# Optimization experiments

Measured on AMD Instinct MI355X. Metric: run time of the kernel, lower is better.

Reference implementation:

```python
import jax, jax.numpy as jnp
import numpy as np

L, D, H, M, NC = 12, 768, 12, 3072, 1000
P, IMG, C = 16, 224, 3
HD = D // H // 2  # 32: diff-attn head dim (2*H query heads of HD, H value heads of 2*HD)
B = 32
N = (IMG // P) ** 2 + 1  # 197
EPS = 1e-5


def _layernorm(x, s, b):
    mu = x.mean(-1, keepdims=True)
    var = ((x - mu) ** 2).mean(-1, keepdims=True)
    return (x - mu) * jax.lax.rsqrt(var + EPS) * s + b


def _rmsnorm(x, s):
    ms = (x * x).mean(-1, keepdims=True)
    return x * jax.lax.rsqrt(ms + EPS) * s


def _diff_attn(x, qw, kw, vw, ow, lq1, lk1, lq2, lk2, sls, lam_init):
    b, n, _ = x.shape
    q = (x @ qw).reshape(b, n, 2 * H, HD)
    k = (x @ kw).reshape(b, n, 2 * H, HD)
    v = (x @ vw).reshape(b, n, H, 2 * HD)
    scores = jnp.einsum('bnhd,bmhd->bhnm', q, k) * (HD ** -0.5)
    attn = jax.nn.softmax(scores, axis=-1)  # [b, 2H, n, n]
    lam = jnp.exp(jnp.sum(lq1 * lk1)) - jnp.exp(jnp.sum(lq2 * lk2)) + lam_init
    attn = attn.reshape(b, H, 2, n, n)
    attn = attn[:, :, 0] - lam * attn[:, :, 1]  # differential attention map
    out = jnp.einsum('bhnm,bmhd->bnhd', attn, v)  # [b, n, H, 2*HD]
    out = _rmsnorm(out, sls) * (1.0 - lam_init)
    return out.reshape(b, n, D) @ ow


def _forward(x, conv_w, conv_b, cls_token, pos_emb,
             ln1_s, ln1_b, q_w, k_w, v_w, o_w, lq1, lk1, lq2, lk2, subln_s,
             ln2_s, ln2_b, w1, b1, w2, b2, lnf_s, lnf_b, head_w, head_b):
    # patch embed: conv stride=patch, then flatten to tokens
    h = jax.lax.conv_general_dilated(x, conv_w, (P, P), 'VALID',
                                     dimension_numbers=('NCHW', 'OIHW', 'NCHW'))
    h = h + conv_b[None, :, None, None]
    bsz = x.shape[0]
    h = h.reshape(bsz, D, -1).transpose(0, 2, 1)  # [B, 196, D]
    h = jnp.concatenate([jnp.broadcast_to(cls_token, (bsz, 1, D)), h], axis=1)
    h = h + pos_emb
    for i in range(L):
        lam_init = 0.8 - 0.6 * np.exp(-0.3 * i)
        a = _diff_attn(_layernorm(h, ln1_s[i], ln1_b[i]), q_w[i], k_w[i], v_w[i], o_w[i],
                       lq1[i], lk1[i], lq2[i], lk2[i], subln_s[i], lam_init)
        h = h + a
        m = _layernorm(h, ln2_s[i], ln2_b[i])
        m = jax.nn.gelu(m @ w1[i] + b1[i]) @ w2[i] + b2[i]
        h = h + m
    h = _layernorm(h, lnf_s, lnf_b)
    return h[:, 0] @ head_w + head_b


def setup_inputs() -> dict:
    key = jax.random.key(0)
    ks = iter(jax.random.split(key, 40))
    def rn(shape, s=0.02):
        return jax.random.normal(next(ks), shape, jnp.float32) * s
    return {
        'x': jax.random.normal(next(ks), (B, C, IMG, IMG), jnp.float32),
        'conv_w': rn((D, C, P, P)), 'conv_b': jnp.zeros((D,), jnp.float32),
        'cls_token': jnp.zeros((1, 1, D), jnp.float32),
        'pos_emb': rn((1, N, D)),
        'ln1_s': jnp.ones((L, D), jnp.float32), 'ln1_b': jnp.zeros((L, D), jnp.float32),
        'q_w': rn((L, D, D)), 'k_w': rn((L, D, D)), 'v_w': rn((L, D, D)), 'o_w': rn((L, D, D)),
        'lq1': rn((L, HD), 0.1), 'lk1': rn((L, HD), 0.1),
        'lq2': rn((L, HD), 0.1), 'lk2': rn((L, HD), 0.1),
        'subln_s': jnp.ones((L, 2 * HD), jnp.float32),
        'ln2_s': jnp.ones((L, D), jnp.float32), 'ln2_b': jnp.zeros((L, D), jnp.float32),
        'w1': rn((L, D, M)), 'b1': jnp.zeros((L, M), jnp.float32),
        'w2': rn((L, M, D)), 'b2': jnp.zeros((L, D), jnp.float32),
        'lnf_s': jnp.ones((D,), jnp.float32), 'lnf_b': jnp.zeros((D,), jnp.float32),
        'head_w': rn((D, NC)), 'head_b': jnp.zeros((NC,), jnp.float32),
    }


def reference(x, conv_w, conv_b, cls_token, pos_emb,
              ln1_s, ln1_b, q_w, k_w, v_w, o_w, lq1, lk1, lq2, lk2, subln_s,
              ln2_s, ln2_b, w1, b1, w2, b2, lnf_s, lnf_b, head_w, head_b):
    return _forward(x, conv_w, conv_b, cls_token, pos_emb,
                    ln1_s, ln1_b, q_w, k_w, v_w, o_w, lq1, lk1, lq2, lk2, subln_s,
                    ln2_s, ln2_b, w1, b1, w2, b2, lnf_s, lnf_b, head_w, head_b)
```

## Files before the change

kernel.cpp:

```cpp
#include <hip/hip_runtime.h>
#include <cmath>


typedef unsigned short u16;
typedef u16 u16x4 __attribute__((ext_vector_type(4)));
typedef u16 u16x8 __attribute__((ext_vector_type(8)));
typedef float fx4 __attribute__((ext_vector_type(4)));
typedef __bf16 bf16x8 __attribute__((ext_vector_type(8)));

#define MROWS 6304
#define MPAD  6400

__device__ __forceinline__ float bf2f(u16 u) {
  union { unsigned int i; float f; } c; c.i = ((unsigned int)u) << 16; return c.f;
}
__device__ __forceinline__ u16 f2bf(float f) {
  union { float f; unsigned int i; } c; c.f = f;
  return (u16)((c.i + 0x7FFFu + ((c.i >> 16) & 1u)) >> 16);
}
__device__ __forceinline__ float gelu_f(float x) {
  float u = 0.7978845608028654f * (x + 0.044715f * x * x * x);
  u = fminf(fmaxf(u, -30.f), 30.f);
  float e = __expf(2.f * u);
  return 0.5f * x * (1.f + (e - 1.f) / (e + 1.f));
}

__device__ __forceinline__ void gload16(const void* g, void* l) {
  __builtin_amdgcn_global_load_lds(
      (const __attribute__((address_space(1))) void*)g,
      (__attribute__((address_space(3))) void*)l, 16, 0, 0);
}

enum { EP_F32 = 0, EP_BF16 = 1, EP_GELU_BF16 = 2, EP_RESID_F32 = 3 };

template<int MODE, bool BIAS>
__global__ __launch_bounds__(256)
void gemm_bf16(const u16* __restrict__ A, const u16* __restrict__ Bt,
               const float* __restrict__ bias, const float* __restrict__ resid,
               void* __restrict__ outp, int M, int N, int K)
{
  __shared__ unsigned char lds[2 * 128 * 64 * 2];
  unsigned char* As = lds;
  unsigned char* Bs = lds + 128 * 64 * 2;
  const int tid = threadIdx.x;
  const int lane = tid & 63, w = tid >> 6;
  const int g = lane >> 4, l = lane & 15;
  const int wr = w >> 1, wc = w & 1;
  const int bm = blockIdx.x * 128, bn = blockIdx.y * 128;

  const int swz_half = ((lane & 7) ^ ((lane >> 3) & 7)) << 3;
  const int srow = 32 * w + (lane >> 3);
  const u16* gA = A + (size_t)(bm + srow) * K + swz_half;
  const u16* gB = Bt + (size_t)(bn + srow) * K + swz_half;
  unsigned char* lA = As + srow * 128 + ((lane & 7) << 4) - (size_t)lane * 16;
  unsigned char* lB = lA + (Bs - As);

  fx4 acc[4][4] = {};

  for (int kt = 0; kt < K; kt += 64) {
    #pragma unroll
    for (int c = 0; c < 4; ++c) {
      gload16(gA + (size_t)(8 * c) * K + kt, lA + (8 * c) * 128);
      gload16(gB + (size_t)(8 * c) * K + kt, lB + (8 * c) * 128);
    }
    __syncthreads();
    #pragma unroll
    for (int kk = 0; kk < 2; ++kk) {
      bf16x8 af[4], bfr[4];
      #pragma unroll
      for (int i = 0; i < 4; ++i) {
        int ar = wr * 64 + i * 16 + l;
        af[i] = *(const bf16x8*)(As + ar * 128 + ((kk * 64 + g * 16) ^ ((ar & 7) << 4)));
        int br = wc * 64 + i * 16 + l;
        bfr[i] = *(const bf16x8*)(Bs + br * 128 + ((kk * 64 + g * 16) ^ ((br & 7) << 4)));
      }
      #pragma unroll
      for (int i = 0; i < 4; ++i)
        #pragma unroll
        for (int j = 0; j < 4; ++j)
          acc[i][j] = __builtin_amdgcn_mfma_f32_16x16x32_bf16(af[i], bfr[j], acc[i][j], 0, 0, 0);
    }
    __syncthreads();
  }
  #pragma unroll
  for (int j = 0; j < 4; ++j) {
    int n = bn + wc * 64 + j * 16 + l;
    float bv = 0.f;
    if (BIAS) bv = bias[n];
    #pragma unroll
    for (int i = 0; i < 4; ++i) {
      int mbase = bm + wr * 64 + i * 16 + g * 4;
      #pragma unroll
      for (int q = 0; q < 4; ++q) {
        int m = mbase + q;
        if (m < M) {
          float v = acc[i][j][q] + bv;
          if (MODE == EP_GELU_BF16) {
            ((u16*)outp)[(size_t)m * N + n] = f2bf(gelu_f(v));
          } else if (MODE == EP_BF16) {
            ((u16*)outp)[(size_t)m * N + n] = f2bf(v);
          } else if (MODE == EP_RESID_F32) {
            ((float*)outp)[(size_t)m * N + n] = resid[(size_t)m * N + n] + v;
          } else {
            ((float*)outp)[(size_t)m * N + n] = v;
          }
        }
      }
    }
  }
}

template<bool OUTF32>
__global__ __launch_bounds__(64)
void layernorm_k(const float* __restrict__ x, const float* __restrict__ s,
                 const float* __restrict__ b, void* __restrict__ outp, size_t in_rstride)
{
  int r = blockIdx.x, lane = threadIdx.x;
  const fx4* xp = (const fx4*)(x + (size_t)r * in_rstride);
  fx4 v[3];
  float sum = 0.f, sq = 0.f;
  #pragma unroll
  for (int j = 0; j < 3; ++j) {
    v[j] = xp[j * 64 + lane];
    #pragma unroll
    for (int e = 0; e < 4; ++e) { sum += v[j][e]; sq += v[j][e] * v[j][e]; }
  }
  #pragma unroll
  for (int off = 32; off; off >>= 1) { sum += __shfl_xor(sum, off); sq += __shfl_xor(sq, off); }
  float mu = sum * (1.f / 768.f);
  float var = sq * (1.f / 768.f) - mu * mu;
  float rs = rsqrtf(var + 1e-5f);
  const fx4* sp = (const fx4*)s;
  const fx4* bp = (const fx4*)b;
  #pragma unroll
  for (int j = 0; j < 3; ++j) {
    fx4 sv = sp[j * 64 + lane], bv = bp[j * 64 + lane];
    if (OUTF32) {
      fx4 o;
      #pragma unroll
      for (int e = 0; e < 4; ++e) o[e] = (v[j][e] - mu) * rs * sv[e] + bv[e];
      *(fx4*)((float*)outp + (size_t)r * 768 + (j * 64 + lane) * 4) = o;
    } else {
      u16x4 o;
      #pragma unroll
      for (int e = 0; e < 4; ++e) o[e] = f2bf((v[j][e] - mu) * rs * sv[e] + bv[e]);
      *(u16x4*)((u16*)outp + (size_t)r * 768 + (j * 64 + lane) * 4) = o;
    }
  }
}

#define KSTR 40
#define VSTR 232
#define DA_LDS (2 * 224 * KSTR * 2 + 64 * VSTR * 2 + 4 * 16 * VSTR * 2)

__global__ __launch_bounds__(256)
void diff_attn(const u16* __restrict__ qkv, const float* __restrict__ lam_p,
               const float* __restrict__ sls, u16* __restrict__ outp, float lam_init)
{
  extern __shared__ char smem[];
  u16* K1s = (u16*)smem;
  u16* K2s = K1s + 224 * KSTR;
  u16* Vt  = K2s + 224 * KSTR;
  const int tid = threadIdx.x;
  const int w = tid >> 6, lane = tid & 63;
  const int g = lane >> 4, l = lane & 15;
  u16* Pw = Vt + 64 * VSTR + w * 16 * VSTR;

  const int bh = blockIdx.x;
  const int b = bh / 12, hh = bh % 12;
  const u16* base = qkv + (size_t)b * 197 * 2304;

  if (tid < 197) {
    const u16* kr = base + (size_t)tid * 2304 + 768 + hh * 64;
    *(u16x8*)(K1s + tid * KSTR + 0)  = *(const u16x8*)(kr + 0);
    *(u16x8*)(K1s + tid * KSTR + 8)  = *(const u16x8*)(kr + 8);
    *(u16x8*)(K1s + tid * KSTR + 16) = *(const u16x8*)(kr + 16);
    *(u16x8*)(K1s + tid * KSTR + 24) = *(const u16x8*)(kr + 24);
    *(u16x8*)(K2s + tid * KSTR + 0)  = *(const u16x8*)(kr + 32);
    *(u16x8*)(K2s + tid * KSTR + 8)  = *(const u16x8*)(kr + 40);
    *(u16x8*)(K2s + tid * KSTR + 16) = *(const u16x8*)(kr + 48);
    *(u16x8*)(K2s + tid * KSTR + 24) = *(const u16x8*)(kr + 56);
    const u16* vr = base + (size_t)tid * 2304 + 1536 + hh * 64;
    #pragma unroll
    for (int jj = 0; jj < 8; ++jj) {
      u16x8 vv = *(const u16x8*)(vr + jj * 8);
      #pragma unroll
      for (int e = 0; e < 8; ++e) Vt[(jj * 8 + e) * VSTR + tid] = vv[e];
    }
  }
  for (int idx = tid; idx < 64 * 27; idx += 256) {
    Vt[(idx / 27) * VSTR + 197 + (idx % 27)] = 0;
  }
  __syncthreads();

  const float lam = lam_p[0];
  const float oscale = 1.f - lam_init;
  const float scale = 0.17677669529663687f;
  const fx4 zero = {};

  for (int qb = w; qb < 13; qb += 4) {
    const int qbase = qb * 16;
    const u16* qrow = base + (size_t)(qbase + l) * 2304 + hh * 64;
    bf16x8 qf1 = *(const bf16x8*)(qrow + g * 8);
    bf16x8 qf2 = *(const bf16x8*)(qrow + 32 + g * 8);

    fx4 s1[14], s2[14];
    #pragma unroll
    for (int t = 0; t < 14; ++t) {
      bf16x8 kf1 = *(const bf16x8*)(K1s + (t * 16 + l) * KSTR + g * 8);
      bf16x8 kf2 = *(const bf16x8*)(K2s + (t * 16 + l) * KSTR + g * 8);
      s1[t] = __builtin_amdgcn_mfma_f32_16x16x32_bf16(qf1, kf1, zero, 0, 0, 0);
      s2[t] = __builtin_amdgcn_mfma_f32_16x16x32_bf16(qf2, kf2, zero, 0, 0, 0);
    }

    float mx1[4] = {-1e30f, -1e30f, -1e30f, -1e30f};
    float mx2[4] = {-1e30f, -1e30f, -1e30f, -1e30f};
    #pragma unroll
    for (int t = 0; t < 14; ++t) {
      bool ok = (t * 16 + l) < 197;
      #pragma unroll
      for (int q = 0; q < 4; ++q) {
        float v1 = ok ? s1[t][q] * scale : -1e30f;
        float v2 = ok ? s2[t][q] * scale : -1e30f;
        s1[t][q] = v1; s2[t][q] = v2;
        mx1[q] = fmaxf(mx1[q], v1); mx2[q] = fmaxf(mx2[q], v2);
      }
    }
    #pragma unroll
    for (int off = 8; off; off >>= 1)
      #pragma unroll
      for (int q = 0; q < 4; ++q) {
        mx1[q] = fmaxf(mx1[q], __shfl_xor(mx1[q], off));
        mx2[q] = fmaxf(mx2[q], __shfl_xor(mx2[q], off));
      }
    float z1[4] = {0, 0, 0, 0}, z2[4] = {0, 0, 0, 0};
    #pragma unroll
    for (int t = 0; t < 14; ++t)
      #pragma unroll
      for (int q = 0; q < 4; ++q) {
        float p1 = __expf(s1[t][q] - mx1[q]);
        float p2 = __expf(s2[t][q] - mx2[q]);
        s1[t][q] = p1; s2[t][q] = p2;
        z1[q] += p1; z2[q] += p2;
      }
    #pragma unroll
    for (int off = 8; off; off >>= 1)
      #pragma unroll
      for (int q = 0; q < 4; ++q) {
        z1[q] += __shfl_xor(z1[q], off);
        z2[q] += __shfl_xor(z2[q], off);
      }
    float r1[4], r2[4];
    #pragma unroll
    for (int q = 0; q < 4; ++q) { r1[q] = 1.f / z1[q]; r2[q] = lam / z2[q]; }

    #pragma unroll
    for (int t = 0; t < 14; ++t)
      #pragma unroll
      for (int q = 0; q < 4; ++q) {
        float pc = s1[t][q] * r1[q] - s2[t][q] * r2[q];
        Pw[(g * 4 + q) * VSTR + t * 16 + l] = f2bf(pc);
      }

    fx4 o[4] = {};
    #pragma unroll
    for (int mt = 0; mt < 7; ++mt) {
      bf16x8 pa = *(const bf16x8*)(Pw + l * VSTR + mt * 32 + g * 8);
      #pragma unroll
      for (int j = 0; j < 4; ++j) {
        bf16x8 vb = *(const bf16x8*)(Vt + (j * 16 + l) * VSTR + mt * 32 + g * 8);
        o[j] = __builtin_amdgcn_mfma_f32_16x16x32_bf16(pa, vb, o[j], 0, 0, 0);
      }
    }

    float ms[4] = {0, 0, 0, 0};
    #pragma unroll
    for (int j = 0; j < 4; ++j)
      #pragma unroll
      for (int q = 0; q < 4; ++q) ms[q] += o[j][q] * o[j][q];
    #pragma unroll
    for (int off = 8; off; off >>= 1)
      #pragma unroll
      for (int q = 0; q < 4; ++q) ms[q] += __shfl_xor(ms[q], off);
    float rr[4];
    #pragma unroll
    for (int q = 0; q < 4; ++q) rr[q] = rsqrtf(ms[q] * (1.f / 64.f) + 1e-5f) * oscale;
    #pragma unroll
    for (int j = 0; j < 4; ++j) {
      float slv = sls[j * 16 + l];
      #pragma unroll
      for (int q = 0; q < 4; ++q) {
        int row = qbase + g * 4 + q;
        if (row < 197)
          outp[(size_t)(b * 197 + row) * 768 + hh * 64 + j * 16 + l] = f2bf(o[j][q] * rr[q] * slv);
      }
    }
  }
}

__global__ __launch_bounds__(256)
void prep_weights(const float* __restrict__ qw, const float* __restrict__ kw,
                  const float* __restrict__ vw, const float* __restrict__ ow,
                  const float* __restrict__ w1, const float* __restrict__ w2,
                  u16* __restrict__ qkvt, u16* __restrict__ ot,
                  u16* __restrict__ w1t, u16* __restrict__ w2t,
                  const float* __restrict__ lq1, const float* __restrict__ lk1,
                  const float* __restrict__ lq2, const float* __restrict__ lk2,
                  float* __restrict__ lam_out, float lam_init)
{
  int bid = blockIdx.x;
  if (bid == 1728) {
    if (threadIdx.x < 64) {
      int lane = threadIdx.x;
      float p1 = lane < 32 ? lq1[lane] * lk1[lane] : 0.f;
      float p2 = lane < 32 ? lq2[lane] * lk2[lane] : 0.f;
      #pragma unroll
      for (int off = 32; off; off >>= 1) { p1 += __shfl_xor(p1, off); p2 += __shfl_xor(p2, off); }
      if (lane == 0) lam_out[0] = __expf(p1) - __expf(p2) + lam_init;
    }
    return;
  }
  const float* src; u16* dst; int Kd, Nd, tx, ty;
  if (bid < 576) {
    int which = bid / 144, t = bid % 144;
    ty = t / 12; tx = t % 12; Kd = 768; Nd = 768;
    src = (which == 0) ? qw : (which == 1) ? kw : (which == 2) ? vw : ow;
    dst = (which < 3) ? (qkvt + (size_t)which * 768 * 768) : ot;
  } else if (bid < 1152) {
    int t = bid - 576; ty = t / 12; tx = t % 12; Kd = 768; Nd = 3072; src = w1; dst = w1t;
  } else {
    int t = bid - 1152; ty = t / 48; tx = t % 48; Kd = 3072; Nd = 768; src = w2; dst = w2t;
  }
  __shared__ u16 tile[64][65];
  int tid2 = threadIdx.x;
  int k0 = tx * 64, n0 = ty * 64;
  #pragma unroll
  for (int j = 0; j < 16; ++j) {
    int idx = j * 256 + tid2;
    int rr = idx >> 6, cc = idx & 63;
    tile[rr][cc] = f2bf(src[(size_t)(k0 + rr) * Nd + n0 + cc]);
  }
  __syncthreads();
  #pragma unroll
  for (int j = 0; j < 16; ++j) {
    int idx = j * 256 + tid2;
    int rr = idx >> 6, cc = idx & 63;
    dst[(size_t)(n0 + rr) * Kd + k0 + cc] = tile[cc][rr];
  }
}

__global__ void convert_cw(const float* __restrict__ src, u16* __restrict__ dst)
{
  int i4 = blockIdx.x * 256 + threadIdx.x;
  fx4 v = *(const fx4*)(src + (size_t)i4 * 4);
  u16x4 o;
  #pragma unroll
  for (int e = 0; e < 4; ++e) o[e] = f2bf(v[e]);
  *(u16x4*)(dst + (size_t)i4 * 4) = o;
}

__global__ void im2col(const float* __restrict__ x, u16* __restrict__ A0)
{
  int i4 = blockIdx.x * 256 + threadIdx.x;
  int base = i4 * 4;
  int r = base / 768, c0 = base % 768;
  int b = r / 196, p = r % 196;
  int py = p / 14, px = p % 14;
  int ch = c0 >> 8;
  int cc = c0 & 255;
  int iy = cc >> 4, ix = cc & 15;
  const float* src = x + (((size_t)(b * 3 + ch) * 224 + py * 16 + iy) * 224 + px * 16 + ix);
  fx4 v = *(const fx4*)src;
  u16x4 o;
  #pragma unroll
  for (int e = 0; e < 4; ++e) o[e] = f2bf(v[e]);
  *(u16x4*)(A0 + base) = o;
}

__global__ void assemble(const float* __restrict__ tmp, const float* __restrict__ conv_b,
                         const float* __restrict__ cls, const float* __restrict__ pos,
                         float* __restrict__ h)
{
  int i4 = blockIdx.x * 256 + threadIdx.x;
  int base = i4 * 4;
  int r = base / 768, d = base % 768;
  int b = r / 197, n = r % 197;
  fx4 pv = *(const fx4*)(pos + (size_t)n * 768 + d);
  fx4 v;
  if (n == 0) {
    v = *(const fx4*)(cls + d);
  } else {
    v = *(const fx4*)(tmp + (size_t)(b * 196 + n - 1) * 768 + d);
    fx4 cb = *(const fx4*)(conv_b + d);
    v = v + cb;
  }
  *(fx4*)(h + (size_t)r * 768 + d) = v + pv;
}

__global__ __launch_bounds__(256)
void head_kernel(const float* __restrict__ ln, const float* __restrict__ hw,
                 const float* __restrict__ hb, float* __restrict__ outp)
{
  int r = blockIdx.x;
  int c = blockIdx.y * 256 + threadIdx.x;
  if (c >= 1000) return;
  const float* lr = ln + (size_t)r * 768;
  float acc = hb[c];
  for (int d = 0; d < 768; ++d)
    acc = fmaf(lr[d], hw[(size_t)d * 1000 + c], acc);
  outp[r * 1000 + c] = acc;
}

extern "C" void kernel_launch(void* const* d_in, const int* in_sizes, int n_in,
                              void* d_out, int out_size, void* d_ws, size_t ws_size,
                              hipStream_t stream)
{
  (void)in_sizes; (void)n_in; (void)out_size; (void)ws_size;
  const float* x      = (const float*)d_in[0];
  const float* conv_w = (const float*)d_in[1];
  const float* conv_b = (const float*)d_in[2];
  const float* cls    = (const float*)d_in[3];
  const float* pos    = (const float*)d_in[4];
  const float* ln1_s  = (const float*)d_in[5];
  const float* ln1_b  = (const float*)d_in[6];
  const float* q_w    = (const float*)d_in[7];
  const float* k_w    = (const float*)d_in[8];
  const float* v_w    = (const float*)d_in[9];
  const float* o_w    = (const float*)d_in[10];
  const float* lq1    = (const float*)d_in[11];
  const float* lk1    = (const float*)d_in[12];
  const float* lq2    = (const float*)d_in[13];
  const float* lk2    = (const float*)d_in[14];
  const float* slsx   = (const float*)d_in[15];
  const float* ln2_s  = (const float*)d_in[16];
  const float* ln2_b  = (const float*)d_in[17];
  const float* w1     = (const float*)d_in[18];
  const float* b1     = (const float*)d_in[19];
  const float* w2     = (const float*)d_in[20];
  const float* b2     = (const float*)d_in[21];
  const float* lnf_s  = (const float*)d_in[22];
  const float* lnf_b  = (const float*)d_in[23];
  const float* head_w = (const float*)d_in[24];
  const float* head_b = (const float*)d_in[25];
  float* out = (float*)d_out;

  char* ws = (char*)d_ws;
  size_t off = 0;
  auto alloc = [&](size_t bytes) { size_t p = off; off += (bytes + 255) & ~(size_t)255; return p; };
  u16*   A_bf  = (u16*)  (ws + alloc((size_t)MPAD * 768 * 2));
  u16*   big   = (u16*)  (ws + alloc((size_t)MPAD * 3072 * 2));
  float* h     = (float*)(ws + alloc((size_t)MROWS * 768 * 4));
  u16*   wqkv  = (u16*)  (ws + alloc((size_t)2304 * 768 * 2));
  u16*   wo    = (u16*)  (ws + alloc((size_t)768 * 768 * 2));
  u16*   w1t   = (u16*)  (ws + alloc((size_t)3072 * 768 * 2));
  u16*   w2t   = (u16*)  (ws + alloc((size_t)768 * 3072 * 2));
  float* lnf_o = (float*)(ws + alloc((size_t)32 * 768 * 4));
  float* lam   = (float*)(ws + alloc(256));
  float* convtmp = (float*)big;
  u16*   cwbf  = w1t;

  hipFuncSetAttribute((const void*)diff_attn,
                      hipFuncAttributeMaxDynamicSharedMemorySize, DA_LDS);

  convert_cw<<<576, 256, 0, stream>>>(conv_w, cwbf);
  im2col<<<4704, 256, 0, stream>>>(x, A_bf);
  gemm_bf16<EP_F32, false><<<dim3(50, 6), 256, 0, stream>>>(
      A_bf, cwbf, nullptr, nullptr, convtmp, 6272, 768, 768);
  assemble<<<4728, 256, 0, stream>>>(convtmp, conv_b, cls, pos, h);

  for (int l = 0; l < 12; ++l) {
    float lam_init = 0.8f - 0.6f * expf(-0.3f * (float)l);
    prep_weights<<<1729, 256, 0, stream>>>(
        q_w + (size_t)l * 589824, k_w + (size_t)l * 589824,
        v_w + (size_t)l * 589824, o_w + (size_t)l * 589824,
        w1 + (size_t)l * 2359296, w2 + (size_t)l * 2359296,
        wqkv, wo, w1t, w2t,
        lq1 + l * 32, lk1 + l * 32, lq2 + l * 32, lk2 + l * 32,
        lam, lam_init);
    layernorm_k<false><<<MROWS, 64, 0, stream>>>(h, ln1_s + l * 768, ln1_b + l * 768, A_bf, (size_t)768);
    gemm_bf16<EP_BF16, false><<<dim3(50, 18), 256, 0, stream>>>(
        A_bf, wqkv, nullptr, nullptr, big, MROWS, 2304, 768);
    diff_attn<<<384, 256, DA_LDS, stream>>>(big, lam, slsx + l * 64, A_bf, lam_init);
    gemm_bf16<EP_RESID_F32, false><<<dim3(50, 6), 256, 0, stream>>>(
        A_bf, wo, nullptr, h, h, MROWS, 768, 768);
    layernorm_k<false><<<MROWS, 64, 0, stream>>>(h, ln2_s + l * 768, ln2_b + l * 768, A_bf, (size_t)768);
    gemm_bf16<EP_GELU_BF16, true><<<dim3(50, 24), 256, 0, stream>>>(
        A_bf, w1t, b1 + l * 3072, nullptr, big, MROWS, 3072, 768);
    gemm_bf16<EP_RESID_F32, true><<<dim3(50, 6), 256, 0, stream>>>(
        big, w2t, b2 + l * 768, h, h, MROWS, 768, 3072);
  }

  layernorm_k<true><<<32, 64, 0, stream>>>(h, lnf_s, lnf_b, lnf_o, (size_t)197 * 768);
  head_kernel<<<dim3(32, 4), 256, 0, stream>>>(lnf_o, head_w, head_b, out);
}
```

Measured before the change: 3.549 ms.

## Double-buffer GEMM LDS tiles and remap workgroups across XCDs

The GEMM kernel now uses two LDS buffers. The next K-tile is prefetched with global_load_lds while MFMAs run on the current tile, so global load latency overlaps compute instead of being exposed before each barrier. The launch grid becomes 1D, and an XCD-aware swizzle maps block IDs so consecutive tiles land on the same XCD, which should improve L2 reuse of A rows. LDS use doubles to 64KB per block, which may reduce occupancy.

```diff
diff --git a/kernel.cpp b/kernel.cpp
--- a/kernel.cpp
+++ b/kernel.cpp
@@ -31,39 +31,52 @@
       (__attribute__((address_space(3))) void*)l, 16, 0, 0);
 }
 
+__device__ __forceinline__ int xcd_swz(int orig, int nwg) {
+  int q = nwg >> 3, r = nwg & 7;
+  int x = orig & 7, i = orig >> 3;
+  return (x < r ? x * (q + 1) : r * (q + 1) + (x - r) * q) + i;
+}
+
 enum { EP_F32 = 0, EP_BF16 = 1, EP_GELU_BF16 = 2, EP_RESID_F32 = 3 };
 
 template<int MODE, bool BIAS>
 __global__ __launch_bounds__(256)
 void gemm_bf16(const u16* __restrict__ A, const u16* __restrict__ Bt,
                const float* __restrict__ bias, const float* __restrict__ resid,
-               void* __restrict__ outp, int M, int N, int K)
-{
-  __shared__ unsigned char lds[2 * 128 * 64 * 2];
-  unsigned char* As = lds;
-  unsigned char* Bs = lds + 128 * 64 * 2;
+               void* __restrict__ outp, int M, int N, int K, int GX)
+{
+  __shared__ unsigned char lds[2][2 * 128 * 64 * 2];
   const int tid = threadIdx.x;
   const int lane = tid & 63, w = tid >> 6;
   const int g = lane >> 4, l = lane & 15;
   const int wr = w >> 1, wc = w & 1;
-  const int bm = blockIdx.x * 128, bn = blockIdx.y * 128;
+  const int wg = xcd_swz(blockIdx.x, gridDim.x);
+  const int bm = (wg % GX) * 128, bn = (wg / GX) * 128;
 
   const int swz_half = ((lane & 7) ^ ((lane >> 3) & 7)) << 3;
   const int srow = 32 * w + (lane >> 3);
   const u16* gA = A + (size_t)(bm + srow) * K + swz_half;
   const u16* gB = Bt + (size_t)(bn + srow) * K + swz_half;
-  unsigned char* lA = As + srow * 128 + ((lane & 7) << 4) - (size_t)lane * 16;
-  unsigned char* lB = lA + (Bs - As);
 
   fx4 acc[4][4] = {};
 
+  auto STAGE = [&](int buf, int kt) {
+    unsigned char* bA = &lds[buf][0] + 4096 * w;
+    unsigned char* bB = bA + 16384;
+    #pragma unroll
+    for (int c = 0; c < 4; ++c) {
+      gload16(gA + (size_t)(8 * c) * K + kt, bA + (8 * c) * 128);
+      gload16(gB + (size_t)(8 * c) * K + kt, bB + (8 * c) * 128);
+    }
+  };
+
+  STAGE(0, 0);
+  __syncthreads();
+  int cur = 0;
   for (int kt = 0; kt < K; kt += 64) {
-    #pragma unroll
-    for (int c = 0; c < 4; ++c) {
-      gload16(gA + (size_t)(8 * c) * K + kt, lA + (8 * c) * 128);
-      gload16(gB + (size_t)(8 * c) * K + kt, lB + (8 * c) * 128);
-    }
-    __syncthreads();
+    if (kt + 64 < K) STAGE(cur ^ 1, kt + 64);
+    const unsigned char* As = &lds[cur][0];
+    const unsigned char* Bs = As + 16384;
     #pragma unroll
     for (int kk = 0; kk < 2; ++kk) {
       bf16x8 af[4], bfr[4];
@@ -81,6 +94,7 @@
           acc[i][j] = __builtin_amdgcn_mfma_f32_16x16x32_bf16(af[i], bfr[j], acc[i][j], 0, 0, 0);
     }
     __syncthreads();
+    cur ^= 1;
   }
   #pragma unroll
   for (int j = 0; j < 4; ++j) {
@@ -464,8 +478,8 @@
 
   convert_cw<<<576, 256, 0, stream>>>(conv_w, cwbf);
   im2col<<<4704, 256, 0, stream>>>(x, A_bf);
-  gemm_bf16<EP_F32, false><<<dim3(50, 6), 256, 0, stream>>>(
-      A_bf, cwbf, nullptr, nullptr, convtmp, 6272, 768, 768);
+  gemm_bf16<EP_F32, false><<<50 * 6, 256, 0, stream>>>(
+      A_bf, cwbf, nullptr, nullptr, convtmp, 6272, 768, 768, 50);
   assemble<<<4728, 256, 0, stream>>>(convtmp, conv_b, cls, pos, h);
 
   for (int l = 0; l < 12; ++l) {
@@ -478,16 +492,16 @@
         lq1 + l * 32, lk1 + l * 32, lq2 + l * 32, lk2 + l * 32,
         lam, lam_init);
     layernorm_k<false><<<MROWS, 64, 0, stream>>>(h, ln1_s + l * 768, ln1_b + l * 768, A_bf, (size_t)768);
-    gemm_bf16<EP_BF16, false><<<dim3(50, 18), 256, 0, stream>>>(
-        A_bf, wqkv, nullptr, nullptr, big, MROWS, 2304, 768);
+    gemm_bf16<EP_BF16, false><<<50 * 18, 256, 0, stream>>>(
+        A_bf, wqkv, nullptr, nullptr, big, MROWS, 2304, 768, 50);
     diff_attn<<<384, 256, DA_LDS, stream>>>(big, lam, slsx + l * 64, A_bf, lam_init);
-    gemm_bf16<EP_RESID_F32, false><<<dim3(50, 6), 256, 0, stream>>>(
-        A_bf, wo, nullptr, h, h, MROWS, 768, 768);
+    gemm_bf16<EP_RESID_F32, false><<<50 * 6, 256, 0, stream>>>(
+        A_bf, wo, nullptr, h, h, MROWS, 768, 768, 50);
     layernorm_k<false><<<MROWS, 64, 0, stream>>>(h, ln2_s + l * 768, ln2_b + l * 768, A_bf, (size_t)768);
-    gemm_bf16<EP_GELU_BF16, true><<<dim3(50, 24), 256, 0, stream>>>(
-        A_bf, w1t, b1 + l * 3072, nullptr, big, MROWS, 3072, 768);
-    gemm_bf16<EP_RESID_F32, true><<<dim3(50, 6), 256, 0, stream>>>(
-        big, w2t, b2 + l * 768, h, h, MROWS, 768, 3072);
+    gemm_bf16<EP_GELU_BF16, true><<<50 * 24, 256, 0, stream>>>(
+        A_bf, w1t, b1 + l * 3072, nullptr, big, MROWS, 3072, 768, 50);
+    gemm_bf16<EP_RESID_F32, true><<<50 * 6, 256, 0, stream>>>(
+        big, w2t, b2 + l * 768, h, h, MROWS, 768, 3072, 50);
   }
 
   layernorm_k<true><<<32, 64, 0, stream>>>(h, lnf_s, lnf_b, lnf_o, (size_t)197 * 768);
```

After: 3.438 ms. 1.03x faster.
